# Optimization experiments

Hardware: AMD Instinct MI355X
Metric: run time of the kernel (lower is better)

The kernel has to match this reference:

```python
import jax, jax.numpy as jnp
import numpy as np

B, N, D = 4, 4096, 1024
HEADS, DIM_HEAD = 16, 64
INNER = HEADS * DIM_HEAD
LN_EPS = 1e-5


def next_fast_len(n):
    # smallest 5-smooth integer >= n (matches scipy.fftpack.next_fast_len)
    while True:
        m = n
        for p in (2, 3, 5):
            while m % p == 0:
                m //= p
        if m == 1:
            return n
        n += 1


def setup_inputs() -> dict:
    key = jax.random.key(0)
    k = jax.random.split(key, 6)
    x = jax.random.normal(k[0], (B, N, D), dtype=jnp.float32)
    gamma = jnp.ones((D,), dtype=jnp.float32)
    beta = jnp.zeros((D,), dtype=jnp.float32)
    alpha = jax.random.normal(k[1], (HEADS,), dtype=jnp.float32)
    w_in = jax.random.normal(k[2], (INNER, D), dtype=jnp.float32) * 0.02
    w_out = jax.random.normal(k[3], (D, INNER), dtype=jnp.float32) * 0.02
    return {"x": x, "gamma": gamma, "beta": beta, "alpha": alpha, "w_in": w_in, "w_out": w_out}


def reference(x, gamma, beta, alpha, w_in, w_out):
    b, n, d = x.shape
    h, dh = HEADS, DIM_HEAD
    # LayerNorm (biased variance, eps=1e-5)
    mu = jnp.mean(x, axis=-1, keepdims=True)
    var = jnp.var(x, axis=-1, keepdims=True)
    xn = (x - mu) * jax.lax.rsqrt(var + LN_EPS) * gamma + beta
    # project_in (no bias), split heads: b n (h d) -> b h n d
    xi = jnp.einsum('bnd,ed->bne', xn, w_in)
    xi = xi.reshape(b, n, h, dh).transpose(0, 2, 1, 3)  # [b,h,n,dh]
    # exponential decay weights per head: alpha * (1-alpha)**flip(arange(n)) -> [h, n]
    a = jax.nn.sigmoid(alpha)[:, None]
    weights = a * (1.0 - a) ** jnp.arange(n - 1, -1, -1, dtype=x.dtype)[None, :]
    # FFT-based causal correlation (conv1d_fft)
    fast_len = next_fast_len(n + n - 1)
    f_x = jnp.fft.rfft(xi, n=fast_len, axis=-2)           # [b,h,L',dh] complex
    f_w = jnp.fft.rfft(weights, n=fast_len, axis=-1)      # [h,L'] complex
    out = jnp.fft.irfft(f_x * jnp.conj(f_w)[None, :, :, None], fast_len, axis=-2)
    out = jnp.roll(out, -1, axis=-2)
    out = out[:, :, fast_len - n:, :]                      # last n positions -> [b,h,n,dh]
    # merge heads and project out
    out = out.transpose(0, 2, 1, 3).reshape(b, n, h * dh)
    return jnp.einsum('bne,de->bnd', out, w_out)
```

## Files before the change

### kernel.cpp

```cpp
#include <hip/hip_runtime.h>
#include <hip/hip_bf16.h>

#define B_ 4
#define N_ 4096
#define D_ 1024
#define H_ 16
#define INNER_ 1024
#define M_ (B_ * N_)
#define CH_ 128
#define CL_ 32

using bf16x8 = __attribute__((ext_vector_type(8))) __bf16;
using f32x4  = __attribute__((ext_vector_type(4))) float;

__device__ __forceinline__ float bf2f(unsigned short v) {
  return __uint_as_float(((unsigned)v) << 16);
}
__device__ __forceinline__ unsigned short f2bf(float f) {
  __hip_bfloat16 h = __float2bfloat16(f);
  return *reinterpret_cast<unsigned short*>(&h);
}
__device__ __forceinline__ float sigm(float x) { return 1.f / (1.f + expf(-x)); }

__device__ __forceinline__ void gload_lds16(const void* g, void* l) {
  __builtin_amdgcn_global_load_lds(
      (const __attribute__((address_space(1))) unsigned int*)g,
      (__attribute__((address_space(3))) unsigned int*)l, 16, 0, 0);
}

__global__ __launch_bounds__(256) void cast_bf16_kernel(
    const float* __restrict__ in, __hip_bfloat16* __restrict__ out, int n4) {
  int i = blockIdx.x * 256 + threadIdx.x;
  if (i >= n4) return;
  float4 v = reinterpret_cast<const float4*>(in)[i];
  ushort4 o;
  o.x = f2bf(v.x); o.y = f2bf(v.y); o.z = f2bf(v.z); o.w = f2bf(v.w);
  reinterpret_cast<ushort4*>(out)[i] = o;
}

__global__ __launch_bounds__(256) void ln_kernel(
    const float* __restrict__ x, const float* __restrict__ gamma,
    const float* __restrict__ beta, __hip_bfloat16* __restrict__ xn) {
  const long row = blockIdx.x;
  const int t = threadIdx.x;
  const float4 v = reinterpret_cast<const float4*>(x + row * D_)[t];
  float s = v.x + v.y + v.z + v.w;
  float s2 = v.x * v.x + v.y * v.y + v.z * v.z + v.w * v.w;
#pragma unroll
  for (int o = 32; o > 0; o >>= 1) {
    s += __shfl_down(s, o);
    s2 += __shfl_down(s2, o);
  }
  __shared__ float red[8];
  const int lane = t & 63, wv = t >> 6;
  if (lane == 0) { red[wv] = s; red[4 + wv] = s2; }
  __syncthreads();
  const float sum = red[0] + red[1] + red[2] + red[3];
  const float sum2 = red[4] + red[5] + red[6] + red[7];
  const float mu = sum * (1.f / D_);
  const float var = sum2 * (1.f / D_) - mu * mu;
  const float rs = rsqrtf(var + 1e-5f);
  const float4 g = reinterpret_cast<const float4*>(gamma)[t];
  const float4 bb = reinterpret_cast<const float4*>(beta)[t];
  ushort4 o;
  o.x = f2bf((v.x - mu) * rs * g.x + bb.x);
  o.y = f2bf((v.y - mu) * rs * g.y + bb.y);
  o.z = f2bf((v.z - mu) * rs * g.z + bb.z);
  o.w = f2bf((v.w - mu) * rs * g.w + bb.w);
  reinterpret_cast<ushort4*>(xn + row * D_)[t] = o;
}

__device__ __forceinline__ void stc(float* p, float v) { *p = v; }
__device__ __forceinline__ void stc(__hip_bfloat16* p, float v) { *p = __float2bfloat16(v); }

template <typename TOUT, int NT>
__global__ __launch_bounds__(512, 2) void gemm256_kernel(
    const __hip_bfloat16* __restrict__ A, const __hip_bfloat16* __restrict__ Bt,
    TOUT* __restrict__ C, int M, int N, int K) {
  static_assert(NT >= 4, "ring needs >=4 tiles");
  __shared__ __align__(16) char lds[131072];
  const int tid = threadIdx.x;
  const int lane = tid & 63;
  const int wave = tid >> 6;

  int wg = blockIdx.y * gridDim.x + blockIdx.x;
  wg = (wg & 7) * 32 + (wg >> 3);
  const int bx = wg & 3;
  const int by = wg >> 2;
  const long bm = (long)by * 256;
  const long bn = (long)bx * 256;

  const int u0  = (tid & 7) ^ ((tid >> 3) & 7);
  const int r0  = 2 * (tid >> 3) + (u0 >> 2);
  const int ck0 = u0 & 3;
  const __hip_bfloat16* sA0 = A  + (bm + r0) * (long)K + ck0 * 8;
  const __hip_bfloat16* sA1 = sA0 + 128l * K;
  const __hip_bfloat16* sB0 = Bt + (bn + r0) * (long)K + ck0 * 8;
  const __hip_bfloat16* sB1 = sB0 + 128l * K;
  char* dbase = (char*)lds + wave * 1024;

  const int wm = wave >> 2;
  const int wn = wave & 3;
  const int fr = lane & 15;
  const int ck = lane >> 4;
  const int pos = (((fr & 1) << 2) | ck) ^ ((fr >> 1) & 7);
  const int laneA = wm * 8192 + (fr >> 1) * 128 + pos * 16;
  const int laneB = 16384 + wn * 4096 + (fr >> 1) * 128 + pos * 16;

  f32x4 acc[8][4] = {};

#define STAGE_A(kt) do { const int _s = (kt) & 3;                         \
    gload_lds16(sA0 + (long)(kt) * 32, dbase + _s * 32768);               \
    gload_lds16(sA1 + (long)(kt) * 32, dbase + _s * 32768 + 8192); } while (0)
#define STAGE_B(kt) do { const int _s = (kt) & 3;                         \
    gload_lds16(sB0 + (long)(kt) * 32, dbase + _s * 32768 + 16384);       \
    gload_lds16(sB1 + (long)(kt) * 32, dbase + _s * 32768 + 24576); } while (0)

  STAGE_A(0); STAGE_B(0);
  STAGE_A(1); STAGE_B(1);
  asm volatile("s_waitcnt vmcnt(4)" ::: "memory");
  __builtin_amdgcn_s_barrier();
  asm volatile("" ::: "memory");

#pragma unroll 4
  for (int t = 0; t < NT; ++t) {
    const char* base = (const char*)lds + (t & 3) * 32768;
    bf16x8 bv[4], av[4];
#pragma unroll
    for (int c = 0; c < 4; ++c) bv[c] = *(const bf16x8*)(base + laneB + c * 1024);
#pragma unroll
    for (int r = 0; r < 4; ++r) av[r] = *(const bf16x8*)(base + laneA + r * 1024);
    if (t + 2 < NT) STAGE_A(t + 2);
    __builtin_amdgcn_s_setprio(1);
#pragma unroll
    for (int r = 0; r < 4; ++r)
#pragma unroll
      for (int c = 0; c < 4; ++c)
        acc[r][c] = __builtin_amdgcn_mfma_f32_16x16x32_bf16(av[r], bv[c], acc[r][c], 0, 0, 0);
    __builtin_amdgcn_s_setprio(0);
#pragma unroll
    for (int r = 0; r < 4; ++r) av[r] = *(const bf16x8*)(base + laneA + (r + 4) * 1024);
    if (t + 2 < NT) STAGE_B(t + 2);
    __builtin_amdgcn_s_setprio(1);
#pragma unroll
    for (int r = 0; r < 4; ++r)
#pragma unroll
      for (int c = 0; c < 4; ++c)
        acc[r + 4][c] = __builtin_amdgcn_mfma_f32_16x16x32_bf16(av[r], bv[c], acc[r + 4][c], 0, 0, 0);
    __builtin_amdgcn_s_setprio(0);
    if (t < NT - 3) asm volatile("s_waitcnt vmcnt(4)" ::: "memory");
    else            asm volatile("s_waitcnt vmcnt(0)" ::: "memory");
    __builtin_amdgcn_s_barrier();
    asm volatile("" ::: "memory");
  }
#undef STAGE_A
#undef STAGE_B

  const int cr = ck * 4;
#pragma unroll
  for (int rf = 0; rf < 8; ++rf)
#pragma unroll
    for (int cf = 0; cf < 4; ++cf)
#pragma unroll
      for (int r = 0; r < 4; ++r) {
        const long row = bm + wm * 128 + rf * 16 + cr + r;
        const long col = bn + wn * 64 + cf * 16 + fr;
        stc(&C[row * (long)N + col], acc[rf][cf][r]);
      }
}

__global__ __launch_bounds__(256) void scan_local_kernel(
    const __hip_bfloat16* __restrict__ xi, __hip_bfloat16* __restrict__ y,
    float* __restrict__ finals, const float* __restrict__ alpha) {
  const int e0 = threadIdx.x * 4;
  const int c = blockIdx.y;
  const int b = blockIdx.z;
  const float a = sigm(alpha[e0 >> 6]);
  const float om = 1.f - a;
  long base = ((long)b * N_ + (long)c * CL_) * INNER_ + e0;
  float y0 = 0.f, y1 = 0.f, y2 = 0.f, y3 = 0.f;
  for (int t = 0; t < CL_; ++t) {
    ushort4 u = *(const ushort4*)(xi + base);
    y0 = om * y0 + a * bf2f(u.x);
    y1 = om * y1 + a * bf2f(u.y);
    y2 = om * y2 + a * bf2f(u.z);
    y3 = om * y3 + a * bf2f(u.w);
    ushort4 o;
    o.x = f2bf(y0); o.y = f2bf(y1); o.z = f2bf(y2); o.w = f2bf(y3);
    *(ushort4*)(y + base) = o;
    base += INNER_;
  }
  float4 f4 = make_float4(y0, y1, y2, y3);
  *reinterpret_cast<float4*>(&finals[((long)b * CH_ + c) * INNER_ + e0]) = f4;
}

__global__ __launch_bounds__(256) void scan_carry_kernel(
    const float* __restrict__ finals, float* __restrict__ carries,
    const float* __restrict__ alpha) {
  const int g = blockIdx.x * 256 + threadIdx.x;
  const int b = g >> 10;
  const int e = g & 1023;
  const float a = sigm(alpha[e >> 6]);
  const float dc = powf(1.f - a, (float)CL_);
  float carry = 0.f;
  for (int c = 0; c < CH_; ++c) {
    const long idx = ((long)b * CH_ + c) * INNER_ + e;
    carries[idx] = carry;
    carry = finals[idx] + dc * carry;
  }
}

__global__ __launch_bounds__(256) void scan_fix_kernel(
    __hip_bfloat16* __restrict__ y, const float* __restrict__ carries,
    const float* __restrict__ alpha) {
  const int t = blockIdx.y;
  const int c = t >> 5;
  if (c == 0) return;
  const int tl = t & 31;
  const int e0 = threadIdx.x * 4;
  const int b = blockIdx.z;
  const float a = sigm(alpha[e0 >> 6]);
  const float om = 1.f - a;
  const float w = exp2f((float)(tl + 1) * log2f(om));
  const float4 cr = *reinterpret_cast<const float4*>(
      &carries[((long)b * CH_ + c) * INNER_ + e0]);
  const long idx = ((long)b * N_ + t) * INNER_ + e0;
  ushort4 u = *(const ushort4*)(y + idx);
  ushort4 o;
  o.x = f2bf(bf2f(u.x) + cr.x * w);
  o.y = f2bf(bf2f(u.y) + cr.y * w);
  o.z = f2bf(bf2f(u.z) + cr.z * w);
  o.w = f2bf(bf2f(u.w) + cr.w * w);
  *(ushort4*)(y + idx) = o;
}

extern "C" void kernel_launch(void* const* d_in, const int* in_sizes, int n_in,
                              void* d_out, int out_size, void* d_ws, size_t ws_size,
                              hipStream_t stream) {
  const float* x     = (const float*)d_in[0];
  const float* gamma = (const float*)d_in[1];
  const float* beta  = (const float*)d_in[2];
  const float* alpha = (const float*)d_in[3];
  const float* w_in  = (const float*)d_in[4];
  const float* w_out = (const float*)d_in[5];
  float* out = (float*)d_out;
  char* ws = (char*)d_ws;

  __hip_bfloat16* xn = (__hip_bfloat16*)ws;
  __hip_bfloat16* wi = (__hip_bfloat16*)(ws + (32l << 20));
  __hip_bfloat16* wo = (__hip_bfloat16*)(ws + (34l << 20));
  float* finals      = (float*)(ws + (36l << 20));
  float* carries     = (float*)(ws + (38l << 20));
  __hip_bfloat16* xi = (__hip_bfloat16*)d_out;

  cast_bf16_kernel<<<1024, 256, 0, stream>>>(w_in, wi, (INNER_ * D_) / 4);
  cast_bf16_kernel<<<1024, 256, 0, stream>>>(w_out, wo, (D_ * INNER_) / 4);

  ln_kernel<<<M_, 256, 0, stream>>>(x, gamma, beta, xn);

  gemm256_kernel<__hip_bfloat16, 32>
      <<<dim3(INNER_ / 256, M_ / 256), 512, 0, stream>>>(xn, wi, xi, M_, INNER_, D_);

  __hip_bfloat16* y = xn;
  scan_local_kernel<<<dim3(1, CH_, B_), 256, 0, stream>>>(xi, y, finals, alpha);
  scan_carry_kernel<<<(B_ * INNER_) / 256, 256, 0, stream>>>(finals, carries, alpha);
  scan_fix_kernel<<<dim3(1, N_, B_), 256, 0, stream>>>(y, carries, alpha);

  gemm256_kernel<float, 32>
      <<<dim3(D_ / 256, M_ / 256), 512, 0, stream>>>(y, wo, out, M_, D_, INNER_);
}
```

Baseline: 143.3 us.

## Fuse chunk-final scan reductions into GEMM epilogue and merge cast with layernorm

The first GEMM epilogue now computes each 32-row chunk's decayed weighted sum (the chunk final state) directly from its accumulators using warp shuffles, so the separate local-scan pass that wrote y and finals disappears. The fix pass is replaced by a single apply pass that reruns the recurrence seeded with the carry, which removes one full read-modify-write of the intermediate. The two weight casts and layernorm are merged into one launch to cut launch overhead. Finals are now computed from fp32 accumulators rather than bf16-rounded values, which slightly changes numerics, and the GEMM epilogue gains extra work and registers.

```diff
diff --git a/kernel.cpp b/kernel.cpp
--- a/kernel.cpp
+++ b/kernel.cpp
@@ -28,20 +28,24 @@
       (__attribute__((address_space(3))) unsigned int*)l, 16, 0, 0);
 }
 
-__global__ __launch_bounds__(256) void cast_bf16_kernel(
-    const float* __restrict__ in, __hip_bfloat16* __restrict__ out, int n4) {
-  int i = blockIdx.x * 256 + threadIdx.x;
-  if (i >= n4) return;
-  float4 v = reinterpret_cast<const float4*>(in)[i];
-  ushort4 o;
-  o.x = f2bf(v.x); o.y = f2bf(v.y); o.z = f2bf(v.z); o.w = f2bf(v.w);
-  reinterpret_cast<ushort4*>(out)[i] = o;
-}
-
-__global__ __launch_bounds__(256) void ln_kernel(
+#define W4_ ((INNER_ * D_) / 4)
+__global__ __launch_bounds__(256) void lncast_kernel(
     const float* __restrict__ x, const float* __restrict__ gamma,
-    const float* __restrict__ beta, __hip_bfloat16* __restrict__ xn) {
-  const long row = blockIdx.x;
+    const float* __restrict__ beta, __hip_bfloat16* __restrict__ xn,
+    const float* __restrict__ wa, const float* __restrict__ wb,
+    __hip_bfloat16* __restrict__ oa, __hip_bfloat16* __restrict__ ob) {
+  if (blockIdx.x < 2048) {
+    int i = blockIdx.x * 256 + threadIdx.x;
+    const float* src = (i < W4_) ? wa : wb;
+    __hip_bfloat16* dst = (i < W4_) ? oa : ob;
+    int j = (i < W4_) ? i : i - W4_;
+    float4 v = reinterpret_cast<const float4*>(src)[j];
+    ushort4 o;
+    o.x = f2bf(v.x); o.y = f2bf(v.y); o.z = f2bf(v.z); o.w = f2bf(v.w);
+    reinterpret_cast<ushort4*>(dst)[j] = o;
+    return;
+  }
+  const long row = blockIdx.x - 2048;
   const int t = threadIdx.x;
   const float4 v = reinterpret_cast<const float4*>(x + row * D_)[t];
   float s = v.x + v.y + v.z + v.w;
@@ -73,10 +77,11 @@
 __device__ __forceinline__ void stc(float* p, float v) { *p = v; }
 __device__ __forceinline__ void stc(__hip_bfloat16* p, float v) { *p = __float2bfloat16(v); }
 
-template <typename TOUT, int NT>
+template <typename TOUT, int NT, bool FUSE>
 __global__ __launch_bounds__(512, 2) void gemm256_kernel(
     const __hip_bfloat16* __restrict__ A, const __hip_bfloat16* __restrict__ Bt,
-    TOUT* __restrict__ C, int M, int N, int K) {
+    TOUT* __restrict__ C, float* __restrict__ finals, const float* __restrict__ alpha,
+    int M, int N, int K) {
   static_assert(NT >= 4, "ring needs >=4 tiles");
   __shared__ __align__(16) char lds[131072];
   const int tid = threadIdx.x;
@@ -167,31 +172,39 @@
         const long col = bn + wn * 64 + cf * 16 + fr;
         stc(&C[row * (long)N + col], acc[rf][cf][r]);
       }
-}
-
-__global__ __launch_bounds__(256) void scan_local_kernel(
-    const __hip_bfloat16* __restrict__ xi, __hip_bfloat16* __restrict__ y,
-    float* __restrict__ finals, const float* __restrict__ alpha) {
-  const int e0 = threadIdx.x * 4;
-  const int c = blockIdx.y;
-  const int b = blockIdx.z;
-  const float a = sigm(alpha[e0 >> 6]);
-  const float om = 1.f - a;
-  long base = ((long)b * N_ + (long)c * CL_) * INNER_ + e0;
-  float y0 = 0.f, y1 = 0.f, y2 = 0.f, y3 = 0.f;
-  for (int t = 0; t < CL_; ++t) {
-    ushort4 u = *(const ushort4*)(xi + base);
-    y0 = om * y0 + a * bf2f(u.x);
-    y1 = om * y1 + a * bf2f(u.y);
-    y2 = om * y2 + a * bf2f(u.z);
-    y3 = om * y3 + a * bf2f(u.w);
-    ushort4 o;
-    o.x = f2bf(y0); o.y = f2bf(y1); o.z = f2bf(y2); o.w = f2bf(y3);
-    *(ushort4*)(y + base) = o;
-    base += INNER_;
-  }
-  float4 f4 = make_float4(y0, y1, y2, y3);
-  *reinterpret_cast<float4*>(&finals[((long)b * CH_ + c) * INNER_ + e0]) = f4;
+
+  if constexpr (FUSE) {
+    const int head = (int)((bn + wn * 64) >> 6);
+    const float a = sigm(alpha[head]);
+    const float lw = log2f(1.f - a);
+    float wgt[2][4];
+#pragma unroll
+    for (int p = 0; p < 2; ++p)
+#pragma unroll
+      for (int r = 0; r < 4; ++r)
+        wgt[p][r] = exp2f((float)(31 - (p * 16 + cr + r)) * lw);
+#pragma unroll
+    for (int q = 0; q < 4; ++q) {
+#pragma unroll
+      for (int cf = 0; cf < 4; ++cf) {
+        float s = 0.f;
+#pragma unroll
+        for (int p = 0; p < 2; ++p)
+#pragma unroll
+          for (int r = 0; r < 4; ++r)
+            s += wgt[p][r] * acc[q * 2 + p][cf][r];
+        s += __shfl_xor(s, 16);
+        s += __shfl_xor(s, 32);
+        if (ck == 0) {
+          const long row0 = bm + wm * 128 + q * 32;
+          const long bb = row0 >> 12;
+          const long cq = (row0 >> 5) & 127;
+          const int e = (int)bn + wn * 64 + cf * 16 + fr;
+          finals[(bb * CH_ + cq) * INNER_ + e] = a * s;
+        }
+      }
+    }
+  }
 }
 
 __global__ __launch_bounds__(256) void scan_carry_kernel(
@@ -210,28 +223,29 @@
   }
 }
 
-__global__ __launch_bounds__(256) void scan_fix_kernel(
-    __hip_bfloat16* __restrict__ y, const float* __restrict__ carries,
-    const float* __restrict__ alpha) {
-  const int t = blockIdx.y;
-  const int c = t >> 5;
-  if (c == 0) return;
-  const int tl = t & 31;
+__global__ __launch_bounds__(256) void scan_apply_kernel(
+    const __hip_bfloat16* __restrict__ xi, __hip_bfloat16* __restrict__ y,
+    const float* __restrict__ carries, const float* __restrict__ alpha) {
   const int e0 = threadIdx.x * 4;
+  const int c = blockIdx.y;
   const int b = blockIdx.z;
   const float a = sigm(alpha[e0 >> 6]);
   const float om = 1.f - a;
-  const float w = exp2f((float)(tl + 1) * log2f(om));
   const float4 cr = *reinterpret_cast<const float4*>(
       &carries[((long)b * CH_ + c) * INNER_ + e0]);
-  const long idx = ((long)b * N_ + t) * INNER_ + e0;
-  ushort4 u = *(const ushort4*)(y + idx);
-  ushort4 o;
-  o.x = f2bf(bf2f(u.x) + cr.x * w);
-  o.y = f2bf(bf2f(u.y) + cr.y * w);
-  o.z = f2bf(bf2f(u.z) + cr.z * w);
-  o.w = f2bf(bf2f(u.w) + cr.w * w);
-  *(ushort4*)(y + idx) = o;
+  float y0 = cr.x, y1 = cr.y, y2 = cr.z, y3 = cr.w;
+  long base = ((long)b * N_ + (long)c * CL_) * INNER_ + e0;
+  for (int t = 0; t < CL_; ++t) {
+    ushort4 u = *(const ushort4*)(xi + base);
+    y0 = om * y0 + a * bf2f(u.x);
+    y1 = om * y1 + a * bf2f(u.y);
+    y2 = om * y2 + a * bf2f(u.z);
+    y3 = om * y3 + a * bf2f(u.w);
+    ushort4 o;
+    o.x = f2bf(y0); o.y = f2bf(y1); o.z = f2bf(y2); o.w = f2bf(y3);
+    *(ushort4*)(y + base) = o;
+    base += INNER_;
+  }
 }
 
 extern "C" void kernel_launch(void* const* d_in, const int* in_sizes, int n_in,
@@ -253,19 +267,17 @@
   float* carries     = (float*)(ws + (38l << 20));
   __hip_bfloat16* xi = (__hip_bfloat16*)d_out;
 
-  cast_bf16_kernel<<<1024, 256, 0, stream>>>(w_in, wi, (INNER_ * D_) / 4);
-  cast_bf16_kernel<<<1024, 256, 0, stream>>>(w_out, wo, (D_ * INNER_) / 4);
-
-  ln_kernel<<<M_, 256, 0, stream>>>(x, gamma, beta, xn);
-
-  gemm256_kernel<__hip_bfloat16, 32>
-      <<<dim3(INNER_ / 256, M_ / 256), 512, 0, stream>>>(xn, wi, xi, M_, INNER_, D_);
+  lncast_kernel<<<2048 + M_, 256, 0, stream>>>(x, gamma, beta, xn, w_in, w_out, wi, wo);
+
+  gemm256_kernel<__hip_bfloat16, 32, true>
+      <<<dim3(INNER_ / 256, M_ / 256), 512, 0, stream>>>(xn, wi, xi, finals, alpha,
+                                                         M_, INNER_, D_);
 
   __hip_bfloat16* y = xn;
-  scan_local_kernel<<<dim3(1, CH_, B_), 256, 0, stream>>>(xi, y, finals, alpha);
   scan_carry_kernel<<<(B_ * INNER_) / 256, 256, 0, stream>>>(finals, carries, alpha);
-  scan_fix_kernel<<<dim3(1, N_, B_), 256, 0, stream>>>(y, carries, alpha);
-
-  gemm256_kernel<float, 32>
-      <<<dim3(D_ / 256, M_ / 256), 512, 0, stream>>>(y, wo, out, M_, D_, INNER_);
-}
+  scan_apply_kernel<<<dim3(1, CH_, B_), 256, 0, stream>>>(xi, y, carries, alpha);
+
+  gemm256_kernel<float, 32, false>
+      <<<dim3(D_ / 256, M_ / 256), 512, 0, stream>>>(y, wo, out, nullptr, nullptr,
+                                                     M_, D_, INNER_);
+}
```

Measured after the change: 123.4 us, median of 2. 1.16x faster.
